# Kernel optimization log

Measured on AMD Instinct MI355X. Metric: run time of the kernel, lower is better.

Reference implementation:

```python
import jax, jax.numpy as jnp
import numpy as np

B, H, T, D = 4, 16, 2048, 128

def setup_inputs() -> dict:
    key = jax.random.key(0)
    kq, kk, kv = jax.random.split(key, 3)
    q = jax.random.normal(kq, (B, H, T, D), dtype=jnp.float32)
    k = jax.random.normal(kk, (B, H, T, D), dtype=jnp.float32)
    v = jax.random.normal(kv, (B, H, T, D), dtype=jnp.float32)
    return {"q": q, "k": k, "v": v}

def reference(q, k, v):
    # scores: [B,H,T,T] = q @ k^T, masked multiplicatively by causal lower-tri ones
    T_ = q.shape[-2]
    mask = jnp.tril(jnp.ones((T_, T_), dtype=q.dtype))  # CausalMulMask
    scores = jnp.einsum('bhid,bhjd->bhij', q, k) * mask
    # no softmax: linear attention, scores @ v
    return jnp.einsum('bhij,bhjd->bhid', scores, v)
```

## Files before the change

### kernel.cpp

```cpp
#include <hip/hip_runtime.h>
#include <stdint.h>

#define SEQ    2048
#define DIM    128
#define CHUNK  128
#define NCHUNK 16
#define NBH    64
#define RECSH  16384
#define KVSH   32768

typedef __attribute__((ext_vector_type(8))) short short8;
typedef __attribute__((ext_vector_type(4))) float floatx4;

#define MFMA(a, b, c) __builtin_amdgcn_mfma_f32_16x16x32_bf16((a), (b), (c), 0, 0, 0)

__device__ __forceinline__ short f2bf(float f) {
  union { float f; uint32_t u; } x; x.f = f;
  uint32_t r = x.u + 0x7fffu + ((x.u >> 16) & 1u);
  return (short)(r >> 16);
}
__device__ __forceinline__ float bf2f(short s) {
  union { uint32_t u; float f; } x;
  x.u = ((uint32_t)(uint16_t)s) << 16;
  return x.f;
}
__device__ __forceinline__ short8 pack8(const float4 a, const float4 b) {
  short8 s;
  s[0] = f2bf(a.x); s[1] = f2bf(a.y); s[2] = f2bf(a.z); s[3] = f2bf(a.w);
  s[4] = f2bf(b.x); s[5] = f2bf(b.y); s[6] = f2bf(b.z); s[7] = f2bf(b.w);
  return s;
}
__device__ __forceinline__ void gload16(const void* g, void* l) {
  __builtin_amdgcn_global_load_lds(
      (const __attribute__((address_space(1))) void*)g,
      (__attribute__((address_space(3))) void*)l, 16, 0, 0);
}
__device__ __forceinline__ int swz(int row, int colsh) {
  return row * 128 + (colsh ^ ((row & 7) << 3));
}

__global__ __launch_bounds__(512, 2) void k_cstate(
    const float* __restrict__ kin, const float* __restrict__ vin,
    short* __restrict__ ws, short* outw) {
  const int blk = blockIdx.x;
  const int bh  = blk & 63;
  const int c   = blk >> 6;
  const size_t base = (size_t)bh * SEQ * DIM + (size_t)c * CHUNK * DIM;
  const float* kc = kin + base;
  const float* vc = vin + base;
  short* rec = outw + (size_t)(bh * NCHUNK + c) * KVSH;

  __shared__ short Kt[128][136];
  __shared__ short Vt[128][136];

  const int tid  = threadIdx.x;
  const int wave = tid >> 6;
  const int lane = tid & 63;
  const int q4   = lane >> 4;
  const int l16  = lane & 15;

  float4 kA[4][2], vA[4][2];
#pragma unroll
  for (int i = 0; i < 4; ++i) {
    const int g = i * 512 + tid;
    const int r = g >> 4, pg = g & 15;
    const float* kp = kc + (size_t)r * DIM + ((pg ^ (r & 7)) << 3);
    kA[i][0] = *(const float4*)kp;
    kA[i][1] = *(const float4*)(kp + 4);
    const float* vp = vc + (size_t)r * DIM + (pg << 3);
    vA[i][0] = *(const float4*)vp;
    vA[i][1] = *(const float4*)(vp + 4);
  }
  __builtin_amdgcn_sched_barrier(0);

#pragma unroll
  for (int i = 0; i < 4; ++i) {
    const int g = i * 512 + tid;
    const int r = g >> 4, pg = g & 15;
    *(short8*)&rec[(size_t)g * 8] = pack8(kA[i][0], kA[i][1]);
    const int ck = (pg ^ (r & 7)) << 3;
    Kt[ck + 0][r] = f2bf(kA[i][0].x); Kt[ck + 1][r] = f2bf(kA[i][0].y);
    Kt[ck + 2][r] = f2bf(kA[i][0].z); Kt[ck + 3][r] = f2bf(kA[i][0].w);
    Kt[ck + 4][r] = f2bf(kA[i][1].x); Kt[ck + 5][r] = f2bf(kA[i][1].y);
    Kt[ck + 6][r] = f2bf(kA[i][1].z); Kt[ck + 7][r] = f2bf(kA[i][1].w);
    const int cv = pg << 3;
    Vt[cv + 0][r] = f2bf(vA[i][0].x); Vt[cv + 1][r] = f2bf(vA[i][0].y);
    Vt[cv + 2][r] = f2bf(vA[i][0].z); Vt[cv + 3][r] = f2bf(vA[i][0].w);
    Vt[cv + 4][r] = f2bf(vA[i][1].x); Vt[cv + 5][r] = f2bf(vA[i][1].y);
    Vt[cv + 6][r] = f2bf(vA[i][1].z); Vt[cv + 7][r] = f2bf(vA[i][1].w);
  }
  __syncthreads();

#pragma unroll
  for (int i = 0; i < 4; ++i) {
    const int g = i * 512 + tid;
    const int r = g >> 4, pg = g & 15;
    *(short8*)&rec[16384 + (size_t)g * 8] =
        *(const short8*)&Vt[r][(pg ^ (r & 7)) << 3];
  }

  floatx4 acc[8];
#pragma unroll
  for (int m = 0; m < 8; ++m)
#pragma unroll
    for (int r = 0; r < 4; ++r) acc[m][r] = 0.f;
#pragma unroll
  for (int ks = 0; ks < 4; ++ks) {
    const short8 bk = *(const short8*)&Kt[wave * 16 + l16][ks * 32 + q4 * 8];
#pragma unroll
    for (int m = 0; m < 8; ++m) {
      const short8 av = *(const short8*)&Vt[m * 16 + l16][ks * 32 + q4 * 8];
      acc[m] = MFMA(av, bk, acc[m]);
    }
  }
  __syncthreads();

  short (*Ss)[136] = (short (*)[136])Kt;
#pragma unroll
  for (int m = 0; m < 8; ++m)
#pragma unroll
    for (int r = 0; r < 4; ++r)
      Ss[m * 16 + q4 * 4 + r][wave * 16 + l16] = f2bf(acc[m][r]);
  __syncthreads();

  short* srec = ws + (size_t)(bh * NCHUNK + c) * RECSH;
#pragma unroll
  for (int i = 0; i < 4; ++i) {
    const int t8  = i * 512 + tid;
    const int row = ((t8 >> 9) << 5) + (((t8 >> 6) & 1) << 4) + (t8 & 15);
    const int col = (((t8 >> 7) & 3) << 5) + (((t8 >> 4) & 3) << 3);
    *(short8*)&srec[(size_t)t8 * 8] = *(const short8*)&Ss[row][col];
  }
}

__global__ __launch_bounds__(256, 4) void k_prefix(short* __restrict__ ws) {
  const int blk = blockIdx.x;
  const int bh  = blk & 63;
  const int p   = blk >> 6;
  const int off = p * 2048 + threadIdx.x * 8;
  short* wb = ws + (size_t)bh * NCHUNK * RECSH;

  float run[8];
#pragma unroll
  for (int s = 0; s < 8; ++s) run[s] = 0.f;
#pragma unroll
  for (int cc = 0; cc < NCHUNK; ++cc) {
    short8* ptr = (short8*)&wb[(size_t)cc * RECSH + off];
    const short8 rv = *ptr;
    short8 ov;
#pragma unroll
    for (int s = 0; s < 8; ++s) ov[s] = f2bf(run[s]);
    *ptr = ov;
#pragma unroll
    for (int s = 0; s < 8; ++s) run[s] += bf2f(rv[s]);
  }
}

__global__ __launch_bounds__(512, 2) void k_out(
    const float* __restrict__ qin, const short* __restrict__ ws,
    float* out) {
  const int blk = blockIdx.x;
  const int bh  = blk & 63;
  const int c   = blk >> 6;
  const size_t base = (size_t)bh * SEQ * DIM + (size_t)c * CHUNK * DIM;
  const float* qc = qin + base;
  float* oc = out + base;
  const short* rec = (const short*)out + (size_t)(bh * NCHUNK + c) * KVSH;

  __shared__ __align__(16) short KVS[49152];

  const int tid  = threadIdx.x;
  const int wave = tid >> 6;
  const int lane = tid & 63;
  const int q4   = lane >> 4;
  const int l16  = lane & 15;

#pragma unroll
  for (int i = 0; i < 8; ++i) {
    const int g = i * 512 + tid;
    gload16(&rec[(size_t)g * 8], &KVS[(size_t)g * 8]);
  }
  const short* sp = ws + (size_t)(bh * NCHUNK + c) * RECSH;
#pragma unroll
  for (int i = 0; i < 4; ++i) {
    const int g = i * 512 + tid;
    gload16(&sp[(size_t)g * 8], &KVS[32768 + (size_t)g * 8]);
  }

  const float* qrow = qc + (size_t)(wave * 16 + l16) * DIM + q4 * 8;
  short8 aq[4];
#pragma unroll
  for (int ks = 0; ks < 4; ++ks)
    aq[ks] = pack8(*(const float4*)(qrow + ks * 32),
                   *(const float4*)(qrow + ks * 32 + 4));
  __syncthreads();

  floatx4 oacc[8];
#pragma unroll
  for (int tn = 0; tn < 8; ++tn)
#pragma unroll
    for (int r = 0; r < 4; ++r) oacc[tn][r] = 0.f;

#pragma unroll
  for (int ks = 0; ks < 4; ++ks)
#pragma unroll
    for (int tn = 0; tn < 8; ++tn) {
      const short8 bs = *(const short8*)
          &KVS[32768 + (tn >> 1) * 4096 + ks * 1024 + (tn & 1) * 512 + lane * 8];
      oacc[tn] = MFMA(aq[ks], bs, oacc[tn]);
    }

  floatx4 sacc[8];
#pragma unroll
  for (int tj = 0; tj < 8; ++tj) {
    if (tj > wave) continue;
#pragma unroll
    for (int r = 0; r < 4; ++r) sacc[tj][r] = 0.f;
#pragma unroll
    for (int ks = 0; ks < 4; ++ks) {
      const short8 bk =
          *(const short8*)&KVS[swz(tj * 16 + l16, ks * 32 + q4 * 8)];
      sacc[tj] = MFMA(aq[ks], bk, sacc[tj]);
    }
  }
  __syncthreads();

#pragma unroll
  for (int tj = 0; tj < 8; ++tj) {
    if (tj > wave) continue;
#pragma unroll
    for (int r = 0; r < 4; ++r) {
      float val = sacc[tj][r];
      if (tj == wave && l16 > q4 * 4 + r) val = 0.f;
      KVS[swz(wave * 16 + q4 * 4 + r, tj * 16 + l16)] = f2bf(val);
    }
  }
  if ((wave & 1) == 0) {
#pragma unroll
    for (int r = 0; r < 4; ++r)
      KVS[swz(wave * 16 + q4 * 4 + r, (wave + 1) * 16 + l16)] = 0;
  }

  const int kst = (wave + 2) >> 1;
  for (int t = 0; t < kst; ++t) {
    const short8 ap =
        *(const short8*)&KVS[swz(wave * 16 + l16, t * 32 + q4 * 8)];
#pragma unroll
    for (int tn = 0; tn < 8; ++tn) {
      const short8 bv =
          *(const short8*)&KVS[16384 + swz(tn * 16 + l16, t * 32 + q4 * 8)];
      oacc[tn] = MFMA(ap, bv, oacc[tn]);
    }
  }

#pragma unroll
  for (int tn = 0; tn < 8; ++tn)
#pragma unroll
    for (int r = 0; r < 4; ++r)
      oc[(size_t)(wave * 16 + q4 * 4 + r) * DIM + tn * 16 + l16] = oacc[tn][r];
}

extern "C" void kernel_launch(void* const* d_in, const int* in_sizes, int n_in,
                              void* d_out, int out_size, void* d_ws, size_t ws_size,
                              hipStream_t stream) {
  const float* q = (const float*)d_in[0];
  const float* k = (const float*)d_in[1];
  const float* v = (const float*)d_in[2];
  float* out = (float*)d_out;
  (void)in_sizes; (void)n_in; (void)out_size; (void)ws_size;
  short* ws = (short*)d_ws;

  hipLaunchKernelGGL(k_cstate, dim3(NBH * NCHUNK), dim3(512), 0, stream,
                     k, v, ws, (short*)d_out);
  hipLaunchKernelGGL(k_prefix, dim3(NBH * 8), dim3(256), 0, stream, ws);
  hipLaunchKernelGGL(k_out, dim3(NBH * NCHUNK), dim3(512), 0, stream,
                     q, ws, out);
}
```

Measured before the change: 273.7 us.

## Store K/V chunk records in MFMA fragment order and reswizzle transposed LDS tiles

The chunk-state kernel now writes the bf16 K and V records to workspace in the exact per-lane MFMA fragment order that the output kernel consumes. The output kernel can then read them with contiguous lane*8 offsets instead of swizzled row addressing. The transposed Kt/Vt LDS tiles get new XOR column swizzles, intended to cut bank conflicts on the scattered scalar transpose stores. In exchange, the global loads of K in k_cstate become less contiguous.

After: 271.4 us. About the same (-0.9%).

```diff
diff --git a/kernel.cpp b/kernel.cpp
--- a/kernel.cpp
+++ b/kernel.cpp
@@ -37,6 +37,12 @@
 }
 __device__ __forceinline__ int swz(int row, int colsh) {
   return row * 128 + (colsh ^ ((row & 7) << 3));
+}
+__device__ __forceinline__ int kcol(int row, int col) {
+  return col ^ (((row >> 3) & 3) << 4);
+}
+__device__ __forceinline__ int vcol(int row, int col) {
+  return col ^ (((row >> 3) & 7) << 3);
 }
 
 __global__ __launch_bounds__(512, 2) void k_cstate(
@@ -62,12 +68,14 @@
   float4 kA[4][2], vA[4][2];
 #pragma unroll
   for (int i = 0; i < 4; ++i) {
-    const int g = i * 512 + tid;
-    const int r = g >> 4, pg = g & 15;
-    const float* kp = kc + (size_t)r * DIM + ((pg ^ (r & 7)) << 3);
+    const int g2 = i * 512 + tid;
+    const int tj = g2 >> 8, ks = (g2 >> 6) & 3, ln = g2 & 63;
+    const float* kp =
+        kc + (size_t)(tj * 16 + (ln & 15)) * DIM + ks * 32 + (ln >> 4) * 8;
     kA[i][0] = *(const float4*)kp;
     kA[i][1] = *(const float4*)(kp + 4);
-    const float* vp = vc + (size_t)r * DIM + (pg << 3);
+    const int g = i * 512 + tid;
+    const float* vp = vc + (size_t)(g >> 4) * DIM + (g & 15) * 8;
     vA[i][0] = *(const float4*)vp;
     vA[i][1] = *(const float4*)(vp + 4);
   }
@@ -75,28 +83,35 @@
 
 #pragma unroll
   for (int i = 0; i < 4; ++i) {
+    const int g2 = i * 512 + tid;
+    const int tj = g2 >> 8, ks = (g2 >> 6) & 3, ln = g2 & 63;
+    *(short8*)&rec[(size_t)g2 * 8] = pack8(kA[i][0], kA[i][1]);
+    const int colb = tj * 16 + (ln & 15);
+    const float* kv = (const float*)&kA[i][0];
+#pragma unroll
+    for (int s = 0; s < 8; ++s) {
+      const int r2 = ks * 32 + (ln >> 4) * 8 + s;
+      Kt[r2][kcol(r2, colb)] = f2bf(kv[s]);
+    }
     const int g = i * 512 + tid;
     const int r = g >> 4, pg = g & 15;
-    *(short8*)&rec[(size_t)g * 8] = pack8(kA[i][0], kA[i][1]);
-    const int ck = (pg ^ (r & 7)) << 3;
-    Kt[ck + 0][r] = f2bf(kA[i][0].x); Kt[ck + 1][r] = f2bf(kA[i][0].y);
-    Kt[ck + 2][r] = f2bf(kA[i][0].z); Kt[ck + 3][r] = f2bf(kA[i][0].w);
-    Kt[ck + 4][r] = f2bf(kA[i][1].x); Kt[ck + 5][r] = f2bf(kA[i][1].y);
-    Kt[ck + 6][r] = f2bf(kA[i][1].z); Kt[ck + 7][r] = f2bf(kA[i][1].w);
-    const int cv = pg << 3;
-    Vt[cv + 0][r] = f2bf(vA[i][0].x); Vt[cv + 1][r] = f2bf(vA[i][0].y);
-    Vt[cv + 2][r] = f2bf(vA[i][0].z); Vt[cv + 3][r] = f2bf(vA[i][0].w);
-    Vt[cv + 4][r] = f2bf(vA[i][1].x); Vt[cv + 5][r] = f2bf(vA[i][1].y);
-    Vt[cv + 6][r] = f2bf(vA[i][1].z); Vt[cv + 7][r] = f2bf(vA[i][1].w);
-  }
-  __syncthreads();
-
-#pragma unroll
-  for (int i = 0; i < 4; ++i) {
-    const int g = i * 512 + tid;
-    const int r = g >> 4, pg = g & 15;
-    *(short8*)&rec[16384 + (size_t)g * 8] =
-        *(const short8*)&Vt[r][(pg ^ (r & 7)) << 3];
+    const float* vv = (const float*)&vA[i][0];
+#pragma unroll
+    for (int s = 0; s < 8; ++s) {
+      const int row = pg * 8 + s;
+      Vt[row][vcol(row, r)] = f2bf(vv[s]);
+    }
+  }
+  __syncthreads();
+
+#pragma unroll
+  for (int i = 0; i < 4; ++i) {
+    const int g3 = i * 512 + tid;
+    const int tdx = g3 >> 6, ln = g3 & 63;
+    const int row = (tdx & 7) * 16 + (ln & 15);
+    const int col = (tdx >> 3) * 32 + (ln >> 4) * 8;
+    *(short8*)&rec[16384 + (size_t)g3 * 8] =
+        *(const short8*)&Vt[row][vcol(row, col)];
   }
 
   floatx4 acc[8];
@@ -104,12 +119,14 @@
   for (int m = 0; m < 8; ++m)
 #pragma unroll
     for (int r = 0; r < 4; ++r) acc[m][r] = 0.f;
+  const int dp = wave * 16 + l16;
 #pragma unroll
   for (int ks = 0; ks < 4; ++ks) {
-    const short8 bk = *(const short8*)&Kt[wave * 16 + l16][ks * 32 + q4 * 8];
+    const short8 bk = *(const short8*)&Kt[dp][kcol(dp, ks * 32 + q4 * 8)];
 #pragma unroll
     for (int m = 0; m < 8; ++m) {
-      const short8 av = *(const short8*)&Vt[m * 16 + l16][ks * 32 + q4 * 8];
+      const int vd = m * 16 + l16;
+      const short8 av = *(const short8*)&Vt[vd][vcol(vd, ks * 32 + q4 * 8)];
       acc[m] = MFMA(av, bk, acc[m]);
     }
   }
@@ -218,8 +235,7 @@
     for (int r = 0; r < 4; ++r) sacc[tj][r] = 0.f;
 #pragma unroll
     for (int ks = 0; ks < 4; ++ks) {
-      const short8 bk =
-          *(const short8*)&KVS[swz(tj * 16 + l16, ks * 32 + q4 * 8)];
+      const short8 bk = *(const short8*)&KVS[(tj * 4 + ks) * 512 + lane * 8];
       sacc[tj] = MFMA(aq[ks], bk, sacc[tj]);
     }
   }
@@ -248,7 +264,7 @@
 #pragma unroll
     for (int tn = 0; tn < 8; ++tn) {
       const short8 bv =
-          *(const short8*)&KVS[16384 + swz(tn * 16 + l16, t * 32 + q4 * 8)];
+          *(const short8*)&KVS[16384 + (t * 8 + tn) * 512 + lane * 8];
       oacc[tn] = MFMA(ap, bv, oacc[tn]);
     }
   }
```
